# Performance work log

Measured on AMD Instinct MI355X. Metric: run time of the kernel, lower is better.

The kernel has to match this reference:

```python
import jax, jax.numpy as jnp
import numpy as np

N = 100_000   # nodes
E = 6_400_000 # edges
R = 90        # relations
NB = 3        # num_blocks


def setup_inputs() -> dict:
    key = jax.random.key(0)
    ks = jax.random.split(key, 10)
    x = jax.random.normal(ks[0], (N, 3), jnp.float32)
    edge_index = jax.random.randint(ks[1], (2, E), 0, N, dtype=jnp.int32)
    edge_type = jax.random.randint(ks[2], (E,), 0, R, dtype=jnp.int32)
    batch = jnp.zeros((N,), jnp.int32)  # single graph, as in source
    p = lambda k, shape: (jax.random.normal(k, shape, jnp.float32) * 0.1)
    # block-diagonal weights: [R, NB, in_b, out_b]
    W1, root1, b1 = p(ks[3], (R, NB, 1, 2)), p(ks[4], (3, 6)), jnp.zeros((6,), jnp.float32)
    W2, root2, b2 = p(ks[5], (R, NB, 2, 1)), p(ks[6], (6, 3)), jnp.zeros((3,), jnp.float32)
    W3, root3, b3 = p(ks[7], (R, NB, 1, 2)), p(ks[8], (3, 6)), jnp.zeros((6,), jnp.float32)
    return dict(x=x, edge_index=edge_index, batch=batch, edge_type=edge_type,
                W1=W1, root1=root1, b1=b1, W2=W2, root2=root2, b2=b2,
                W3=W3, root3=root3, b3=b3)


def _rgcn(x, src, dst, edge_type, W, root, bias, aggr):
    # block-diagonal per-relation transform of gathered source features
    nb, in_b, out_b = W.shape[1], W.shape[2], W.shape[3]
    xb = x[src].reshape(-1, nb, in_b)                      # [E, NB, in_b]
    msg = jnp.einsum('ebi,ebio->ebo', xb, W[edge_type])    # [E, NB, out_b]
    msg = msg.reshape(-1, nb * out_b)                      # [E, out]
    if aggr == 'mean':
        # per-(dst node, relation) normalization, as in FastRGCNConv
        comb = dst * R + edge_type                         # [E]
        cnt = jax.ops.segment_sum(jnp.ones((msg.shape[0],), msg.dtype), comb,
                                  num_segments=N * R)      # [N*R]
        msg = msg / jnp.clip(cnt[comb], 1.0)[:, None]
    agg = jax.ops.segment_sum(msg, dst, num_segments=N)    # [N, out]
    return agg + x @ root + bias


def reference(x, edge_index, batch, edge_type, W1, root1, b1, W2, root2, b2, W3, root3, b3):
    src, dst = edge_index[0], edge_index[1]
    h = jax.nn.relu(_rgcn(x, src, dst, edge_type, W1, root1, b1, 'mean'))
    # dropout is identity in eval mode
    h = jax.nn.relu(_rgcn(h, src, dst, edge_type, W2, root2, b2, 'add'))
    h = jax.nn.relu(_rgcn(h, src, dst, edge_type, W3, root3, b3, 'mean'))
    # global mean pool over batch (single graph here, kept general)
    num_graphs = 1
    s = jax.ops.segment_sum(h, batch, num_segments=num_graphs)
    c = jax.ops.segment_sum(jnp.ones((h.shape[0],), h.dtype), batch, num_segments=num_graphs)
    pooled = s / jnp.clip(c, 1.0)[:, None]
    return jax.nn.log_softmax(pooled, axis=1)
```

## Files before the change

kernel.cpp:

```cpp
#include <hip/hip_runtime.h>


#define NREL   90
#define BSH    7
#define BNODES 128
#define NBINS  1024
#define NB2    784
#define GCH    8704
#define KPT    17
#define SPK    11056
#define CAPB   10496
#define NV4    6
#define STAGE  9088
#define LPD    16
#define SENT   0xFFFFFFFFu

__device__ __forceinline__ float frelu(float v) { return v > 0.0f ? v : 0.0f; }

__launch_bounds__(512)
__global__ void group_k(const float* __restrict__ x, float4* __restrict__ x4,
                        int N, int gNp,
                        const int* __restrict__ src, const int* __restrict__ dst,
                        const int* __restrict__ et, int* __restrict__ gcount,
                        unsigned* __restrict__ regions, int E) {
    int tid = threadIdx.x;
    if (blockIdx.x < gNp) {
        int i = blockIdx.x * 512 + tid;
        if (i < N) x4[i] = make_float4(x[3 * i], x[3 * i + 1], x[3 * i + 2], 0.0f);
        return;
    }
    __shared__ int s_cur[NB2];
    __shared__ int s_pend[NB2];
    __shared__ int s_off[NB2];
    __shared__ unsigned s_pack[SPK];
    int chunk = blockIdx.x - gNp;
    int e0 = chunk * GCH;
    int cnt = min(GCH, E - e0);
    for (int i = tid; i < NB2; i += 512) s_pend[i] = 0;
    __syncthreads();
    unsigned rec[KPT];
    int bkt[KPT];
#pragma unroll
    for (int k = 0; k < KPT; k++) {
        int q = tid + k * 512;
        if (q < cnt) {
            int e = e0 + q;
            int d = dst[e];
            bkt[k] = d >> BSH;
            rec[k] = (unsigned)src[e] | ((unsigned)et[e] << 17) |
                     ((unsigned)(d & (BNODES - 1)) << 24);
            atomicAdd(&s_pend[bkt[k]], 1);
        } else bkt[k] = -1;
    }
    __syncthreads();
    if (tid < 49) {
        int loc[16];
        int s = 0;
        int b0 = tid * 16;
#pragma unroll
        for (int k = 0; k < 16; k++) {
            int plen = (s_pend[b0 + k] + 3) & ~3;
            loc[k] = plen; s += plen;
        }
        int inc = s;
#pragma unroll
        for (int off = 1; off < 64; off <<= 1) {
            int u = __shfl_up(inc, off);
            if (tid >= off) inc += u;
        }
        int run = inc - s;
#pragma unroll
        for (int k = 0; k < 16; k++) {
            s_cur[b0 + k] = run;
            run += loc[k];
            s_pend[b0 + k] = run;
        }
    }
    __syncthreads();
    int T = s_pend[NB2 - 1];
    for (int b = tid; b < NB2; b += 512) {
        int st = s_cur[b];
        int plen = s_pend[b] - st;
        if (plen > 0) {
            int gb = atomicAdd(&gcount[b], plen);
            if (gb + plen <= CAPB) {
                s_off[b] = gb - st;
            } else {
                s_off[b] = 0x40000000;
                unsigned* reg = regions + (size_t)b * CAPB;
                for (int j = min(gb, CAPB); j < CAPB; j++) reg[j] = SENT;
            }
        } else s_off[b] = 0x40000000;
    }
    for (int i = tid; i < T; i += 512) s_pack[i] = SENT;
    __syncthreads();
#pragma unroll
    for (int k = 0; k < KPT; k++) {
        if (bkt[k] >= 0) {
            int p = atomicAdd(&s_cur[bkt[k]], 1);
            s_pack[p] = rec[k];
        }
    }
    __syncthreads();
    int nv = T >> 2;
    for (int i4 = tid; i4 < nv; i4 += 512) {
        int i = i4 << 2;
        int lo = 0, hi = NB2 - 1;
        while (lo < hi) {
            int mid = (lo + hi) >> 1;
            if (s_pend[mid] > i) hi = mid; else lo = mid + 1;
        }
        int loc = s_off[lo] + i;
        if (loc < CAPB) {
            uint4 v = make_uint4(s_pack[i], s_pack[i + 1],
                                 s_pack[i + 2], s_pack[i + 3]);
            *(uint4*)(regions + (size_t)lo * CAPB + loc) = v;
        }
    }
}

__launch_bounds__(512)
__global__ void sortb_l1_k(const int* __restrict__ gcount, unsigned* regions,
                           int2* __restrict__ rowseg,
                           const float4* __restrict__ x4, const float* __restrict__ W,
                           const float* __restrict__ root, const float* __restrict__ bias,
                           float4* __restrict__ h1p, int N) {
    __shared__ unsigned stage32[STAGE];
    __shared__ unsigned hist8w[BNODES * 90 / 4];
    __shared__ int hh[BNODES], base_[BNODES];
    __shared__ float4 w4[NREL * 2];
    int tid = threadIdx.x, b = blockIdx.x;
    for (int i = tid; i < BNODES * 90 / 4; i += 512) hist8w[i] = 0u;
    for (int i = tid; i < NREL * 2; i += 512) {
        int r = i >> 1;
        w4[i] = (i & 1) ? make_float4(W[r * 6 + 4], W[r * 6 + 5], 0.f, 0.f)
                        : make_float4(W[r * 6], W[r * 6 + 1], W[r * 6 + 2], W[r * 6 + 3]);
    }
    __syncthreads();
    int fill = gcount[b];
    if (fill > CAPB) fill = CAPB;
    const uint4* reg4 = (const uint4*)(regions + (size_t)b * CAPB);
    int nv = fill >> 2;
    uint4 rec4[NV4];
#define HIST1(P) if ((P) != SENT) { \
        unsigned bi_ = ((P) >> 24) * 90u + (((P) >> 17) & 127u); \
        atomicAdd(&hist8w[bi_ >> 2], 1u << ((bi_ & 3) << 3)); }
#pragma unroll
    for (int k = 0; k < NV4; k++) {
        int i4 = tid + k * 512;
        if (i4 < nv) {
            uint4 v = reg4[i4];
            rec4[k] = v;
            HIST1(v.x); HIST1(v.y); HIST1(v.z); HIST1(v.w);
        } else {
            rec4[k] = make_uint4(SENT, SENT, SENT, SENT);
        }
    }
    __syncthreads();
    if (tid < 64) {
        int wbase = 45 * tid;
        unsigned run = 0;
        int hhA = 0;
#pragma unroll
        for (int w = 0; w < 45; w++) {
            unsigned v = hist8w[wbase + w];
            unsigned nvw = 0;
#pragma unroll
            for (int j = 0; j < 4; j++) {
                if (w * 4 + j == 90) { hhA = (int)run; run = 0; }
                unsigned c = (v >> (8 * j)) & 0xFFu;
                nvw |= (run & 0xFFu) << (8 * j);
                run += c;
            }
            hist8w[wbase + w] = nvw;
        }
        int c0 = hhA, c1 = (int)run;
        hh[2 * tid] = c0; hh[2 * tid + 1] = c1;
        int s = c0 + c1;
        int inc = s;
#pragma unroll
        for (int off = 1; off < 64; off <<= 1) {
            int u = __shfl_up(inc, off);
            if (tid >= off) inc += u;
        }
        int run2 = inc - s;
        base_[2 * tid] = run2;
        base_[2 * tid + 1] = run2 + c0;
    }
    __syncthreads();
    int cntv = base_[BNODES - 1] + hh[BNODES - 1];
    if (tid < BNODES) {
        int d = (b << BSH) + tid;
        if (d < N) {
            int beg = base_[tid];
            int end = beg + hh[tid];
            if (end > cntv) end = cntv;
            rowseg[d] = make_int2(b * CAPB + beg, b * CAPB + end);
        }
    }
#define PLACE1(P) if ((P) != SENT) { \
        unsigned dL_ = (P) >> 24; \
        unsigned bi_ = dL_ * 90u + (((P) >> 17) & 127u); \
        unsigned old_ = atomicAdd(&hist8w[bi_ >> 2], 1u << ((bi_ & 3) << 3)); \
        int pos_ = base_[dL_] + (int)((old_ >> ((bi_ & 3) << 3)) & 0xFFu); \
        if (pos_ < STAGE) stage32[pos_] = (P); }
#pragma unroll
    for (int k = 0; k < NV4; k++) {
        PLACE1(rec4[k].x); PLACE1(rec4[k].y); PLACE1(rec4[k].z); PLACE1(rec4[k].w);
    }
    __syncthreads();
    const unsigned char* h8 = (const unsigned char*)hist8w;
    unsigned* regw = regions + (size_t)b * CAPB;
    int grp = tid >> 4, l16 = tid & 15;
#pragma unroll
    for (int rd = 0; rd < 4; rd++) {
        int dL = grp + rd * 32;
        int segb = base_[dL];
        int sege = segb + hh[dL];
        if (sege > cntv) sege = cntv;
        float a0 = 0, a1 = 0, a2 = 0, a3 = 0, a4 = 0, a5 = 0;
        for (int q = segb + l16; q < sege; q += 16) {
            unsigned p = stage32[q];
            unsigned rel = (p >> 17) & 127u;
            unsigned bi = dL * 90u + rel;
            unsigned c = (unsigned)h8[bi] - (rel ? (unsigned)h8[bi - 1] : 0u);
            regw[q] = (p & 0x00FFFFFFu) | (c << 24);
            float r = __builtin_amdgcn_rcpf((float)c);
            float4 xv = x4[p & 0x1FFFFu];
            unsigned rel2 = rel * 2u;
            float4 wa = w4[rel2], wb = w4[rel2 + 1];
            float x0 = xv.x * r, x1 = xv.y * r, x2 = xv.z * r;
            a0 += x0 * wa.x; a1 += x0 * wa.y;
            a2 += x1 * wa.z; a3 += x1 * wa.w;
            a4 += x2 * wb.x; a5 += x2 * wb.y;
        }
#pragma unroll
        for (int off = 8; off > 0; off >>= 1) {
            a0 += __shfl_down(a0, off); a1 += __shfl_down(a1, off); a2 += __shfl_down(a2, off);
            a3 += __shfl_down(a3, off); a4 += __shfl_down(a4, off); a5 += __shfl_down(a5, off);
        }
        if (l16 == 0) {
            int d = (b << BSH) + dL;
            if (d < N) {
                float4 xv = x4[d];
                float o[6] = {a0, a1, a2, a3, a4, a5};
#pragma unroll
                for (int j = 0; j < 6; j++)
                    o[j] = frelu(o[j] + xv.x * root[j] + xv.y * root[6 + j] +
                                 xv.z * root[12 + j] + bias[j]);
                h1p[d * 2]     = make_float4(o[0], o[1], o[2], o[3]);
                h1p[d * 2 + 1] = make_float4(o[4], o[5], 0.0f, 0.0f);
            }
        }
    }
}

__launch_bounds__(256)
__global__ void l2_g(const int2* __restrict__ rowseg, const unsigned* __restrict__ sorted,
                     const float4* __restrict__ h1p, const float* __restrict__ W,
                     const float* __restrict__ root, const float* __restrict__ bias,
                     float4* __restrict__ h2p, int N) {
    __shared__ float4 w4[NREL * 2];
    for (int i = threadIdx.x; i < NREL * 2; i += 256) {
        int r = i >> 1;
        w4[i] = (i & 1) ? make_float4(W[r * 6 + 4], W[r * 6 + 5], 0.f, 0.f)
                        : make_float4(W[r * 6], W[r * 6 + 1], W[r * 6 + 2], W[r * 6 + 3]);
    }
    __syncthreads();
    int grp = threadIdx.x >> 4, l16 = threadIdx.x & 15;
    int d = blockIdx.x * LPD + grp;
    if (d >= N) return;
    int2 sg = rowseg[d];
    int beg = sg.x, end = sg.y;
    float a0 = 0, a1 = 0, a2 = 0;
    for (int i0 = beg + l16; i0 < end; i0 += 64) {
        unsigned p[4];
        float sc[4];
        float4 ha[4], hb[4];
#pragma unroll
        for (int k = 0; k < 4; k++) {
            int i = i0 + k * 16;
            int ic = i < end ? i : end - 1;
            p[k] = sorted[ic];
            sc[k] = i < end ? 1.0f : 0.0f;
        }
#pragma unroll
        for (int k = 0; k < 4; k++) {
            unsigned s = p[k] & 0x1FFFFu;
            ha[k] = h1p[2 * s]; hb[k] = h1p[2 * s + 1];
        }
#pragma unroll
        for (int k = 0; k < 4; k++) {
            unsigned rel2 = ((p[k] >> 17) & 127u) * 2u;
            float4 wa = w4[rel2], wb = w4[rel2 + 1];
            float m0 = ha[k].x * wa.x + ha[k].y * wa.y;
            float m1 = ha[k].z * wa.z + ha[k].w * wa.w;
            float m2 = hb[k].x * wb.x + hb[k].y * wb.y;
            a0 += sc[k] * m0; a1 += sc[k] * m1; a2 += sc[k] * m2;
        }
    }
#pragma unroll
    for (int off = 8; off > 0; off >>= 1) {
        a0 += __shfl_down(a0, off); a1 += __shfl_down(a1, off); a2 += __shfl_down(a2, off);
    }
    if (l16 == 0) {
        float4 ha = h1p[2 * d], hb = h1p[2 * d + 1];
        float hv[6] = {ha.x, ha.y, ha.z, ha.w, hb.x, hb.y};
        float o[3] = {a0, a1, a2};
#pragma unroll
        for (int j = 0; j < 3; j++) {
            float v = o[j] + bias[j];
#pragma unroll
            for (int k = 0; k < 6; k++) v += hv[k] * root[k * 3 + j];
            o[j] = frelu(v);
        }
        h2p[d] = make_float4(o[0], o[1], o[2], 0.0f);
    }
}

__launch_bounds__(256)
__global__ void l3_g(const int2* __restrict__ rowseg, const unsigned* __restrict__ sorted,
                     const float4* __restrict__ h2p, const float* __restrict__ W,
                     const float* __restrict__ root, const float* __restrict__ bias,
                     const int* __restrict__ batch, float* __restrict__ partials, int N) {
    __shared__ float4 w4[NREL * 2];
    __shared__ float redsm[LPD][8];
    for (int i = threadIdx.x; i < NREL * 2; i += 256) {
        int r = i >> 1;
        w4[i] = (i & 1) ? make_float4(W[r * 6 + 4], W[r * 6 + 5], 0.f, 0.f)
                        : make_float4(W[r * 6], W[r * 6 + 1], W[r * 6 + 2], W[r * 6 + 3]);
    }
    __syncthreads();
    int grp = threadIdx.x >> 4, l16 = threadIdx.x & 15;
    int d = blockIdx.x * LPD + grp;
    float a0 = 0, a1 = 0, a2 = 0, a3 = 0, a4 = 0, a5 = 0;
    if (d < N) {
        int2 sg = rowseg[d];
        int beg = sg.x, end = sg.y;
        for (int i0 = beg + l16; i0 < end; i0 += 64) {
            unsigned p[4];
            float sc[4];
            float4 xv[4];
#pragma unroll
            for (int k = 0; k < 4; k++) {
                int i = i0 + k * 16;
                int ic = i < end ? i : end - 1;
                p[k] = sorted[ic];
                sc[k] = i < end ? 1.0f : 0.0f;
            }
#pragma unroll
            for (int k = 0; k < 4; k++) xv[k] = h2p[p[k] & 0x1FFFFu];
#pragma unroll
            for (int k = 0; k < 4; k++) {
                float r = sc[k] * __builtin_amdgcn_rcpf((float)(p[k] >> 24));
                unsigned rel2 = ((p[k] >> 17) & 127u) * 2u;
                float4 wa = w4[rel2], wb = w4[rel2 + 1];
                float x0 = xv[k].x * r, x1 = xv[k].y * r, x2 = xv[k].z * r;
                a0 += x0 * wa.x; a1 += x0 * wa.y;
                a2 += x1 * wa.z; a3 += x1 * wa.w;
                a4 += x2 * wb.x; a5 += x2 * wb.y;
            }
        }
    }
#pragma unroll
    for (int off = 8; off > 0; off >>= 1) {
        a0 += __shfl_down(a0, off); a1 += __shfl_down(a1, off); a2 += __shfl_down(a2, off);
        a3 += __shfl_down(a3, off); a4 += __shfl_down(a4, off); a5 += __shfl_down(a5, off);
    }
    if (l16 == 0) {
        float v[7] = {0, 0, 0, 0, 0, 0, 0};
        if (d < N && batch[d] == 0) {
            float4 xv = h2p[d];
            float o[6] = {a0, a1, a2, a3, a4, a5};
#pragma unroll
            for (int j = 0; j < 6; j++)
                v[j] = frelu(o[j] + xv.x * root[j] + xv.y * root[6 + j] +
                             xv.z * root[12 + j] + bias[j]);
            v[6] = 1.0f;
        }
#pragma unroll
        for (int k = 0; k < 7; k++) redsm[grp][k] = v[k];
    }
    __syncthreads();
    if (threadIdx.x < 7) {
        float t = 0;
#pragma unroll
        for (int g = 0; g < LPD; g++) t += redsm[g][threadIdx.x];
        partials[(size_t)blockIdx.x * 8 + threadIdx.x] = t;
    }
}

__global__ void pool_finalize(const float* __restrict__ partials, int nb,
                              float* __restrict__ out) {
    float v[7] = {0, 0, 0, 0, 0, 0, 0};
    for (int b = threadIdx.x; b < nb; b += blockDim.x) {
#pragma unroll
        for (int k = 0; k < 7; k++) v[k] += partials[(size_t)b * 8 + k];
    }
#pragma unroll
    for (int off = 32; off > 0; off >>= 1) {
#pragma unroll
        for (int k = 0; k < 7; k++) v[k] += __shfl_down(v[k], off);
    }
    __shared__ float sm[16][8];
    int wv = threadIdx.x >> 6, lane = threadIdx.x & 63;
    if (lane == 0) {
#pragma unroll
        for (int k = 0; k < 7; k++) sm[wv][k] = v[k];
    }
    __syncthreads();
    if (threadIdx.x == 0) {
        float t[7] = {0, 0, 0, 0, 0, 0, 0};
        int nw = blockDim.x >> 6;
        for (int q = 0; q < nw; q++) {
#pragma unroll
            for (int k = 0; k < 7; k++) t[k] += sm[q][k];
        }
        float c = t[6] < 1.0f ? 1.0f : t[6];
        float p[6], m = -1e30f;
#pragma unroll
        for (int j = 0; j < 6; j++) { p[j] = t[j] / c; m = fmaxf(m, p[j]); }
        float s = 0.0f;
#pragma unroll
        for (int j = 0; j < 6; j++) s += expf(p[j] - m);
        float lse = m + logf(s);
#pragma unroll
        for (int j = 0; j < 6; j++) out[j] = p[j] - lse;
    }
}

extern "C" void kernel_launch(void* const* d_in, const int* in_sizes, int n_in,
                              void* d_out, int out_size, void* d_ws, size_t ws_size,
                              hipStream_t stream) {
    const float* x     = (const float*)d_in[0];
    const int*   ei    = (const int*)d_in[1];
    const int*   batch = (const int*)d_in[2];
    const int*   etype = (const int*)d_in[3];
    const float* W1    = (const float*)d_in[4];
    const float* root1 = (const float*)d_in[5];
    const float* b1    = (const float*)d_in[6];
    const float* W2    = (const float*)d_in[7];
    const float* root2 = (const float*)d_in[8];
    const float* b2    = (const float*)d_in[9];
    const float* W3    = (const float*)d_in[10];
    const float* root3 = (const float*)d_in[11];
    const float* b3    = (const float*)d_in[12];

    const int N = in_sizes[0] / 3;
    const int E = in_sizes[1] / 2;
    const int* src = ei;
    const int* dst = ei + E;
    const int gG = (E + GCH - 1) / GCH;
    const int NBUCK = (N + BNODES - 1) >> BSH;
    const int gL = (N + LPD - 1) / LPD;

    char* ws = (char*)d_ws;
    size_t off = 0;
    auto alloc = [&](size_t bytes) -> void* {
        void* p = ws + off;
        off += (bytes + 255) & ~(size_t)255;
        return p;
    };
    int*      gcount  = (int*)     alloc(NBINS * sizeof(int));
    size_t zero_bytes = off;
    unsigned* regions = (unsigned*)alloc((size_t)NBUCK * CAPB * sizeof(unsigned));
    int2*     rowseg  = (int2*)    alloc((size_t)N * sizeof(int2));
    float4*   x4      = (float4*)  alloc((size_t)N * sizeof(float4));
    float4*   h1p     = (float4*)  alloc((size_t)N * 2 * sizeof(float4));
    float4*   h2p     = (float4*)  alloc((size_t)N * sizeof(float4));
    float*    partials = (float*)  alloc((size_t)gL * 8 * sizeof(float));

    hipMemsetAsync(d_ws, 0, zero_bytes, stream);

    const int gNp = (N + 511) / 512;

    group_k<<<gNp + gG, 512, 0, stream>>>(x, x4, N, gNp, src, dst, etype,
                                          gcount, regions, E);
    sortb_l1_k<<<NBUCK, 512, 0, stream>>>(gcount, regions, rowseg,
                                          x4, W1, root1, b1, h1p, N);
    l2_g<<<gL, 256, 0, stream>>>(rowseg, regions, h1p, W2, root2, b2, h2p, N);
    l3_g<<<gL, 256, 0, stream>>>(rowseg, regions, h2p, W3, root3, b3, batch, partials, N);
    pool_finalize<<<1, 1024, 0, stream>>>(partials, gL, (float*)d_out);
}
```

Baseline: 284.1 us.

## Coalesce sorted-record writeback via LDS staging and simplify per-node histogram scan

Sorted edge records are written back into the shared stage buffer during layer-1 accumulation, then copied out to global memory in a separate coalesced uint4 pass instead of scattered 32-bit global stores. All global loads are issued before the histogram atomics to improve memory-level parallelism. The per-block byte-histogram prefix scan is rewritten as 128 threads each scanning their own 90-bin row serially, replacing the packed 64-thread word scan. Adds an extra barrier and a copy pass, clamps segment bounds to the stage capacity, and the serial byte scan may cause LDS bank conflicts.

```diff
diff --git a/kernel.cpp b/kernel.cpp
--- a/kernel.cpp
+++ b/kernel.cpp
@@ -142,40 +142,33 @@
     const uint4* reg4 = (const uint4*)(regions + (size_t)b * CAPB);
     int nv = fill >> 2;
     uint4 rec4[NV4];
+#pragma unroll
+    for (int k = 0; k < NV4; k++) {
+        int i4 = tid + k * 512;
+        rec4[k] = (i4 < nv) ? reg4[i4] : make_uint4(SENT, SENT, SENT, SENT);
+    }
 #define HIST1(P) if ((P) != SENT) { \
         unsigned bi_ = ((P) >> 24) * 90u + (((P) >> 17) & 127u); \
         atomicAdd(&hist8w[bi_ >> 2], 1u << ((bi_ & 3) << 3)); }
 #pragma unroll
     for (int k = 0; k < NV4; k++) {
-        int i4 = tid + k * 512;
-        if (i4 < nv) {
-            uint4 v = reg4[i4];
-            rec4[k] = v;
-            HIST1(v.x); HIST1(v.y); HIST1(v.z); HIST1(v.w);
-        } else {
-            rec4[k] = make_uint4(SENT, SENT, SENT, SENT);
-        }
+        HIST1(rec4[k].x); HIST1(rec4[k].y); HIST1(rec4[k].z); HIST1(rec4[k].w);
+    }
+    __syncthreads();
+    unsigned char* h8w = (unsigned char*)hist8w;
+    if (tid < BNODES) {
+        unsigned run = 0;
+        int rbase = tid * 90;
+        for (int k = 0; k < 90; k++) {
+            unsigned c = h8w[rbase + k];
+            h8w[rbase + k] = (unsigned char)run;
+            run += c;
+        }
+        hh[tid] = (int)run;
     }
     __syncthreads();
     if (tid < 64) {
-        int wbase = 45 * tid;
-        unsigned run = 0;
-        int hhA = 0;
-#pragma unroll
-        for (int w = 0; w < 45; w++) {
-            unsigned v = hist8w[wbase + w];
-            unsigned nvw = 0;
-#pragma unroll
-            for (int j = 0; j < 4; j++) {
-                if (w * 4 + j == 90) { hhA = (int)run; run = 0; }
-                unsigned c = (v >> (8 * j)) & 0xFFu;
-                nvw |= (run & 0xFFu) << (8 * j);
-                run += c;
-            }
-            hist8w[wbase + w] = nvw;
-        }
-        int c0 = hhA, c1 = (int)run;
-        hh[2 * tid] = c0; hh[2 * tid + 1] = c1;
+        int c0 = hh[2 * tid], c1 = hh[2 * tid + 1];
         int s = c0 + c1;
         int inc = s;
 #pragma unroll
@@ -189,11 +182,13 @@
     }
     __syncthreads();
     int cntv = base_[BNODES - 1] + hh[BNODES - 1];
+    if (cntv > STAGE) cntv = STAGE;
     if (tid < BNODES) {
         int d = (b << BSH) + tid;
         if (d < N) {
             int beg = base_[tid];
             int end = beg + hh[tid];
+            if (beg > cntv) beg = cntv;
             if (end > cntv) end = cntv;
             rowseg[d] = make_int2(b * CAPB + beg, b * CAPB + end);
         }
@@ -210,7 +205,6 @@
     }
     __syncthreads();
     const unsigned char* h8 = (const unsigned char*)hist8w;
-    unsigned* regw = regions + (size_t)b * CAPB;
     int grp = tid >> 4, l16 = tid & 15;
 #pragma unroll
     for (int rd = 0; rd < 4; rd++) {
@@ -224,7 +218,7 @@
             unsigned rel = (p >> 17) & 127u;
             unsigned bi = dL * 90u + rel;
             unsigned c = (unsigned)h8[bi] - (rel ? (unsigned)h8[bi - 1] : 0u);
-            regw[q] = (p & 0x00FFFFFFu) | (c << 24);
+            stage32[q] = (p & 0x00FFFFFFu) | (c << 24);
             float r = __builtin_amdgcn_rcpf((float)c);
             float4 xv = x4[p & 0x1FFFFu];
             unsigned rel2 = rel * 2u;
@@ -252,6 +246,18 @@
                 h1p[d * 2 + 1] = make_float4(o[4], o[5], 0.0f, 0.0f);
             }
         }
+    }
+    __syncthreads();
+    unsigned* regw = regions + (size_t)b * CAPB;
+    int nv2 = (cntv + 3) >> 2;
+    for (int i4 = tid; i4 < nv2; i4 += 512) {
+        int i = i4 << 2;
+        uint4 v;
+        v.x = stage32[i];
+        v.y = (i + 1 < cntv) ? stage32[i + 1] : SENT;
+        v.z = (i + 2 < cntv) ? stage32[i + 2] : SENT;
+        v.w = (i + 3 < cntv) ? stage32[i + 3] : SENT;
+        *(uint4*)(regw + i) = v;
     }
 }
 
```

Result: no change. 283.0 us (-0.4%).
